# Kernel optimization log

Measured on AMD Instinct MI355X. Metric: run time of the kernel, lower is better.

## Reference

```python
import jax, jax.numpy as jnp
import numpy as np

D_MODEL, D_STATE, D_CONV, D_INNER, DT_RANK, K = 96, 16, 3, 192, 6, 4
B, H, W = 1, 64, 64


def setup_inputs() -> dict:
    key = jax.random.key(0)
    ks = jax.random.split(key, 10)
    x = jax.random.normal(ks[0], (B, H, W, D_MODEL), jnp.float32)
    in_proj_w = jax.random.normal(ks[1], (2 * D_INNER, D_MODEL), jnp.float32) * 0.02
    conv_w = jax.random.normal(ks[2], (D_INNER, 1, D_CONV, D_CONV), jnp.float32) * 0.1
    conv_b = jnp.zeros((D_INNER,), jnp.float32)
    x_proj_w = jax.random.normal(ks[3], (K, DT_RANK + 2 * D_STATE, D_INNER), jnp.float32) * 0.02
    dt_std = DT_RANK ** -0.5
    dt_w = jax.random.uniform(ks[4], (K, D_INNER, DT_RANK), jnp.float32, -dt_std, dt_std)
    # dt bias init: inv-softplus of dt ~ logUniform(1e-3, 1e-1)
    u = jax.random.uniform(ks[5], (K, D_INNER), jnp.float32)
    dt = jnp.exp(u * (np.log(0.1) - np.log(0.001)) + np.log(0.001)).clip(1e-4)
    dt_b = dt + jnp.log(-jnp.expm1(-dt))
    A_logs = jnp.log(jnp.broadcast_to(jnp.arange(1, D_STATE + 1, dtype=jnp.float32), (K * D_INNER, D_STATE)))
    Ds = jnp.ones((K * D_INNER,), jnp.float32)
    ln_g = jnp.ones((D_INNER,), jnp.float32)
    ln_b = jnp.zeros((D_INNER,), jnp.float32)
    out_proj_w = jax.random.normal(ks[6], (D_MODEL, D_INNER), jnp.float32) * 0.02
    return dict(x=x, in_proj_w=in_proj_w, conv_w=conv_w, conv_b=conv_b, x_proj_w=x_proj_w,
                dt_w=dt_w, dt_b=dt_b, A_logs=A_logs, Ds=Ds, ln_g=ln_g, ln_b=ln_b,
                out_proj_w=out_proj_w)


def _ss2d(x, in_proj_w, conv_w, conv_b, x_proj_w, dt_w, dt_b, A_logs, Ds, ln_g, ln_b, out_proj_w):
    b, h, w, c = x.shape
    L = h * w
    d = conv_w.shape[0]            # d_inner
    n = A_logs.shape[1]            # d_state
    r = dt_w.shape[2]              # dt_rank
    # in_proj + split
    xz = jnp.einsum('bhwc,ec->bhwe', x, in_proj_w)
    xx, z = xz[..., :d], xz[..., d:]
    # depthwise conv (NCHW) + SiLU
    xc = xx.transpose(0, 3, 1, 2)
    pad = (D_CONV - 1) // 2
    xc = jax.lax.conv_general_dilated(xc, conv_w, (1, 1), [(pad, pad), (pad, pad)],
                                      feature_group_count=d) + conv_b[None, :, None, None]
    xc = jax.nn.silu(xc)
    # 4 scan directions: HW, WH, and their reverses
    x_hw = xc.reshape(b, d, L)
    x_wh = xc.transpose(0, 1, 3, 2).reshape(b, d, L)
    xs = jnp.stack([x_hw, x_wh, x_hw[..., ::-1], x_wh[..., ::-1]], axis=1)  # (b,K,d,L)
    x_dbl = jnp.einsum('bkdl,kcd->bkcl', xs, x_proj_w)
    dts, Bs, Cs = x_dbl[:, :, :r], x_dbl[:, :, r:r + n], x_dbl[:, :, r + n:]
    dts = jnp.einsum('bkrl,kdr->bkdl', dts, dt_w)
    delta = jax.nn.softplus(dts + dt_b[None, :, :, None])        # (b,K,d,L)
    A = -jnp.exp(A_logs).reshape(K, d, n)
    # time-major scanned inputs
    dA = jnp.exp(jnp.einsum('bkdl,kdn->lbkdn', delta, A))        # (L,b,K,d,n)
    dBu = jnp.einsum('bkdl,bknl,bkdl->lbkdn', delta, Bs, xs)
    Ct = Cs.transpose(3, 0, 1, 2)                                # (L,b,K,n)
    def step(hst, inp):
        dA_t, dBu_t, C_t = inp
        hst = dA_t * hst + dBu_t
        return hst, jnp.einsum('bkdn,bkn->bkd', hst, C_t)
    h0 = jnp.zeros((b, K, d, n), jnp.float32)
    _, ys = jax.lax.scan(step, h0, (dA, dBu, Ct))                # ys: (L,b,K,d)
    out_y = ys.transpose(1, 2, 3, 0) + xs * Ds.reshape(K, d)[None, :, :, None]
    # recombine directions
    inv = out_y[:, 2:4][..., ::-1]
    y1 = out_y[:, 0]
    y2 = inv[:, 0]
    wh = out_y[:, 1].reshape(b, d, w, h).transpose(0, 1, 3, 2).reshape(b, d, L)
    invwh = inv[:, 1].reshape(b, d, w, h).transpose(0, 1, 3, 2).reshape(b, d, L)
    y = (y1 + y2 + wh + invwh).transpose(0, 2, 1).reshape(b, h, w, d)
    # LayerNorm (eps=1e-5, torch default)
    mu = y.mean(-1, keepdims=True)
    var = ((y - mu) ** 2).mean(-1, keepdims=True)
    y = (y - mu) * jax.lax.rsqrt(var + 1e-5) * ln_g + ln_b
    y = y * jax.nn.silu(z)
    return jnp.einsum('bhwd,cd->bhwc', y, out_proj_w)


def reference(x, in_proj_w, conv_w, conv_b, x_proj_w, dt_w, dt_b, A_logs, Ds, ln_g, ln_b, out_proj_w):
    return _ss2d(x, in_proj_w, conv_w, conv_b, x_proj_w, dt_w, dt_b, A_logs, Ds, ln_g, ln_b, out_proj_w)
```

## Files before the change

### kernel.cpp

```cpp
#include <hip/hip_runtime.h>
#include <hip/hip_bf16.h>

#define LL 4096
#define DM 96
#define DI 192
#define NS 16
#define RK 6
#define RKP 8
#define KD 4
#define CPROJ 38
#define NC (KD*DI*NS)
#define PT 32
#define WS 196
#define OT 16
#define L2E 1.44269504f

__device__ __forceinline__ float b2f(__hip_bfloat16 v){ return __bfloat162float(v); }

__device__ __forceinline__ int detect_bf16(const unsigned short* __restrict__ xh, int tid, int* sflag){
  if (tid < 64){
    unsigned short u = xh[2*tid];
    int e = (u >> 7) & 0xFF;
    int sane = (e >= 107 && e <= 131) ? 1 : 0;
    unsigned long long m = __ballot(sane);
    if (tid == 0) *sflag = (__popcll(m) >= 32) ? 1 : 0;
  }
  return 0;
}

struct P12 { const void* p[12]; };
__global__ void k_convert_all(P12 ptrs, float* __restrict__ dst) {
  const int off[13] = {0,393216,430080,431808,432000,461184,465792,466560,
                       478848,479616,479808,480000,498432};
  __shared__ int sflag;
  detect_bf16((const unsigned short*)ptrs.p[0], threadIdx.x, &sflag);
  __syncthreads();
  int f = sflag;
  int i = blockIdx.x * 256 + threadIdx.x;
  if (i >= 498432) return;
  int j = 0;
  #pragma unroll
  for (int s = 1; s < 12; s++) if (i >= off[s]) j = s;
  int e = i - off[j];
  if (f) dst[i] = b2f(((const __hip_bfloat16*)ptrs.p[j])[e]);
  else   dst[i] = ((const float*)ptrs.p[j])[e];
}

__global__ void k_inproj(const float* __restrict__ x,
                         const float* __restrict__ w,
                         float* __restrict__ xx, float* __restrict__ z) {
  __shared__ float xr[8*DM];
  int l0 = blockIdx.x * 8;
  int tid = threadIdx.x;
  for (int i = tid; i < 8*DM; i += 384) xr[i] = x[l0*DM + i];
  __syncthreads();
  int e = tid;
  float acc[8];
  #pragma unroll
  for (int i=0;i<8;i++) acc[i]=0.f;
  const float* wr = w + e*DM;
  for (int c=0;c<DM;c++){
    float wv = wr[c];
    #pragma unroll
    for (int i=0;i<8;i++) acc[i] = fmaf(wv, xr[i*DM+c], acc[i]);
  }
  if (e < DI) {
    #pragma unroll
    for (int i=0;i<8;i++) xx[(l0+i)*DI + e] = acc[i];
  } else {
    int e2 = e - DI;
    #pragma unroll
    for (int i=0;i<8;i++) z[(l0+i)*DI + e2] = acc[i];
  }
}

__global__ void k_conv(const float* __restrict__ xx,
                       const float* __restrict__ cw,
                       const float* __restrict__ cb,
                       float* __restrict__ xc,
                       float* __restrict__ xct) {
  int l = blockIdx.x;
  int d = threadIdx.x;
  int h = l >> 6, w = l & 63;
  float acc = cb[d];
  #pragma unroll
  for (int ki=0; ki<3; ki++){
    int hh = h + ki - 1;
    if ((unsigned)hh >= 64u) continue;
    #pragma unroll
    for (int kj=0;kj<3;kj++){
      int wj = w + kj - 1;
      if ((unsigned)wj >= 64u) continue;
      acc = fmaf(cw[d*9 + ki*3 + kj], xx[(hh*64+wj)*DI + d], acc);
    }
  }
  float v = acc / (1.f + __expf(-acc));
  xc[l*DI + d] = v;
  xct[(((w<<6)|h))*DI + d] = v;
}

__device__ __forceinline__ int dir_map(int k, int t){
  if (k==0) return t;
  if (k==1) return ((t&63)<<6) | (t>>6);
  if (k==2) return 4095 - t;
  int u = 4095 - t; return ((u&63)<<6) | (u>>6);
}

__global__ void __launch_bounds__(256) k_proj(const float* __restrict__ xc,
                       const float* __restrict__ xpw,
                       float* __restrict__ dts,
                       float* __restrict__ Bb, float* __restrict__ Cb,
                       float* __restrict__ yacc_hw, float* __restrict__ yacc_wh) {
  __shared__ float wl[CPROJ*WS];
  __shared__ float xs[PT*WS];
  int b = blockIdx.x;
  int k = b >> 7;
  int t_base = (b & 127) * PT;
  int tid = threadIdx.x;
  if (k < 2){
    float4* yz = (float4*)((k==0 ? yacc_hw : yacc_wh) + (size_t)t_base*DI);
    for (int idx = tid; idx < PT*DI/4; idx += 256)
      yz[idx] = make_float4(0.f,0.f,0.f,0.f);
  }
  for (int idx = tid; idx < CPROJ*DI; idx += 256){
    int cc = idx / DI, j = idx - cc*DI;
    wl[cc*WS + j] = xpw[(k*CPROJ + cc)*DI + j];
  }
  for (int idx = tid; idx < PT*DI; idx += 256){
    int tt = idx / DI, j = idx - tt*DI;
    xs[tt*WS + j] = xc[dir_map(k, t_base + tt)*DI + j];
  }
  __syncthreads();
  int tg = tid & 7;
  int ty = tid >> 3;
  int cc0 = ty;
  int has2 = (ty + 32 < CPROJ);
  int cc1 = has2 ? (ty + 32) : ty;
  float a0x=0.f,a0y=0.f,a0z=0.f,a0w=0.f;
  float a1x=0.f,a1y=0.f,a1z=0.f,a1w=0.f;
  const float4* w0p = (const float4*)&wl[cc0*WS];
  const float4* w1p = (const float4*)&wl[cc1*WS];
  const float4* x0p = (const float4*)&xs[(tg     )*WS];
  const float4* x1p = (const float4*)&xs[(tg +  8)*WS];
  const float4* x2p = (const float4*)&xs[(tg + 16)*WS];
  const float4* x3p = (const float4*)&xs[(tg + 24)*WS];
  #pragma unroll 4
  for (int jc = 0; jc < DI/4; jc++){
    float4 w0 = w0p[jc], w1 = w1p[jc];
    float4 x0 = x0p[jc], x1 = x1p[jc], x2 = x2p[jc], x3 = x3p[jc];
    a0x = fmaf(w0.x,x0.x,fmaf(w0.y,x0.y,fmaf(w0.z,x0.z,fmaf(w0.w,x0.w,a0x))));
    a0y = fmaf(w0.x,x1.x,fmaf(w0.y,x1.y,fmaf(w0.z,x1.z,fmaf(w0.w,x1.w,a0y))));
    a0z = fmaf(w0.x,x2.x,fmaf(w0.y,x2.y,fmaf(w0.z,x2.z,fmaf(w0.w,x2.w,a0z))));
    a0w = fmaf(w0.x,x3.x,fmaf(w0.y,x3.y,fmaf(w0.z,x3.z,fmaf(w0.w,x3.w,a0w))));
    a1x = fmaf(w1.x,x0.x,fmaf(w1.y,x0.y,fmaf(w1.z,x0.z,fmaf(w1.w,x0.w,a1x))));
    a1y = fmaf(w1.x,x1.x,fmaf(w1.y,x1.y,fmaf(w1.z,x1.z,fmaf(w1.w,x1.w,a1y))));
    a1z = fmaf(w1.x,x2.x,fmaf(w1.y,x2.y,fmaf(w1.z,x2.z,fmaf(w1.w,x2.w,a1z))));
    a1w = fmaf(w1.x,x3.x,fmaf(w1.y,x3.y,fmaf(w1.z,x3.z,fmaf(w1.w,x3.w,a1w))));
  }
  float accs0[4] = {a0x,a0y,a0z,a0w};
  float accs1[4] = {a1x,a1y,a1z,a1w};
  #pragma unroll
  for (int i=0;i<4;i++){
    int t = t_base + tg + 8*i;
    size_t kt = (size_t)k*LL + t;
    {
      int cc = cc0; float v = accs0[i];
      if (cc < RK)            dts[kt*RKP + cc] = v;
      else if (cc < RK+NS)    Bb [kt*NS + (cc-RK)] = v;
      else                    Cb [kt*NS + (cc-RK-NS)] = v;
    }
    if (has2){
      int cc = ty + 32; float v = accs1[i];
      if (cc < RK+NS)         Bb [kt*NS + (cc-RK)] = v;
      else                    Cb [kt*NS + (cc-RK-NS)] = v;
    }
  }
}

template<int CHB>
__global__ void __launch_bounds__(256) k_scan1(
                      const float* __restrict__ xc_hw,
                      const float* __restrict__ xc_wh,
                      const float* __restrict__ dts,
                      const float* __restrict__ Bbuf,
                      const float* __restrict__ Cbuf,
                      const float* __restrict__ A_logs,
                      const float* __restrict__ dtw,
                      const float* __restrict__ dtb,
                      float* __restrict__ Pb, float* __restrict__ Hb,
                      float* __restrict__ SDb,
                      float* __restrict__ yacc_hw, float* __restrict__ yacc_wh) {
  constexpr int CS = LL >> CHB;
  int b = blockIdx.x;
  int c = b & ((1<<CHB)-1);
  int kg = b >> CHB;
  int k = kg / 3, dg3 = kg - k*3;
  int tid = threadIdx.x;
  int dl = tid >> 2, nq = tid & 3;
  int d = dg3*64 + dl;
  int kd = k*DI + d;
  float4 Al = *(const float4*)&A_logs[kd*NS + nq*4];
  float A0 = -__expf(Al.x)*L2E, A1 = -__expf(Al.y)*L2E;
  float A2 = -__expf(Al.z)*L2E, A3 = -__expf(Al.w)*L2E;
  float bt = dtb[kd];
  float w0 = dtw[kd*RK+0], w1 = dtw[kd*RK+1], w2 = dtw[kd*RK+2];
  float w3 = dtw[kd*RK+3], w4 = dtw[kd*RK+4], w5 = dtw[kd*RK+5];
  const float* dr = dts + ((size_t)k*LL + c*CS)*RKP;
  const float4* bp = (const float4*)(Bbuf + ((size_t)k*LL + c*CS)*NS) + nq;
  const float4* cp = (const float4*)(Cbuf + ((size_t)k*LL + c*CS)*NS) + nq;
  const float* xbase = (k & 1) ? xc_wh : xc_hw;
  float* ybase = (k & 1) ? yacc_wh : yacc_hw;
  int l0 = (k < 2) ? (c*CS) : (4095 - c*CS);
  int lstep = (k < 2) ? DI : -DI;
  const float* xp = xbase + (size_t)l0*DI + d;
  float* yp = ybase + (size_t)l0*DI + d;
  float* sdp = SDb + ((size_t)k*LL + c*CS)*DI + d;
  float h0=0.f,h1=0.f,h2=0.f,h3=0.f, cumD=0.f;
  #pragma unroll
  for (int s=0; s<CS; s++){
    float4 lo = *(const float4*)(dr + s*RKP);
    float4 hi = *(const float4*)(dr + s*RKP + 4);
    float v = bt;
    v = fmaf(w0, lo.x, v); v = fmaf(w1, lo.y, v); v = fmaf(w2, lo.z, v);
    v = fmaf(w3, lo.w, v); v = fmaf(w4, hi.x, v); v = fmaf(w5, hi.y, v);
    float sp = (v > 20.f) ? v : __logf(1.f + __expf(v));
    cumD += sp;
    float sx = sp * xp[(ptrdiff_t)s*lstep];
    float4 bv = bp[s*4];
    float4 cv = cp[s*4];
    float a;
    a = exp2f(sp*A0); h0 = fmaf(a, h0, sx*bv.x);
    a = exp2f(sp*A1); h1 = fmaf(a, h1, sx*bv.y);
    a = exp2f(sp*A2); h2 = fmaf(a, h2, sx*bv.z);
    a = exp2f(sp*A3); h3 = fmaf(a, h3, sx*bv.w);
    float y = h0*cv.x + h1*cv.y + h2*cv.z + h3*cv.w;
    y += __shfl_xor(y, 1, 64);
    y += __shfl_xor(y, 2, 64);
    if (nq == 0){
      atomicAdd(&yp[(ptrdiff_t)s*lstep], y);
      sdp[s*DI] = cumD;
    }
  }
  int base = c*NC + kd*NS + nq*4;
  *(float4*)&Pb[base] = make_float4(exp2f(A0*cumD), exp2f(A1*cumD),
                                    exp2f(A2*cumD), exp2f(A3*cumD));
  *(float4*)&Hb[base] = make_float4(h0,h1,h2,h3);
}

template<int CHB>
__global__ void __launch_bounds__(256) k_scan2(
                      const float* __restrict__ Pb, float* __restrict__ Hb) {
  constexpr int CH = 1 << CHB;
  int idx = blockIdx.x*256 + threadIdx.x;
  float h = 0.f;
  #pragma unroll 8
  for (int c=0;c<CH;c++){
    float P = Pb[c*NC + idx];
    float Hc = Hb[c*NC + idx];
    Hb[c*NC + idx] = h;
    h = fmaf(P, h, Hc);
  }
}

template<int CHB>
__global__ void __launch_bounds__(192) k_corr(
                      const float* __restrict__ Cbuf,
                      const float* __restrict__ A_logs,
                      const float* __restrict__ Hb,
                      const float* __restrict__ SDb,
                      float* __restrict__ yacc_hw, float* __restrict__ yacc_wh) {
  constexpr int CS = LL >> CHB;
  int b = blockIdx.x;
  int k = b >> CHB;
  int c = b & ((1<<CHB)-1);
  if (c == 0) return;
  int t0 = c*CS;
  int d = threadIdx.x;
  int kd = k*DI + d;
  __shared__ float cs[CS*NS];
  for (int i = d; i < CS*NS; i += 192)
    cs[i] = Cbuf[((size_t)k*LL + t0)*NS + i];
  float A2[16], he[16];
  {
    const float4* ap = (const float4*)&A_logs[kd*NS];
    const float4* hp = (const float4*)&Hb[c*NC + kd*NS];
    #pragma unroll
    for (int i=0;i<4;i++){
      float4 av = ap[i];
      A2[4*i+0] = -__expf(av.x)*L2E; A2[4*i+1] = -__expf(av.y)*L2E;
      A2[4*i+2] = -__expf(av.z)*L2E; A2[4*i+3] = -__expf(av.w)*L2E;
      *(float4*)&he[4*i] = hp[i];
    }
  }
  __syncthreads();
  float* ybase = (k & 1) ? yacc_wh : yacc_hw;
  int l0 = (k < 2) ? t0 : (4095 - t0);
  int lstep = (k < 2) ? DI : -DI;
  float* yp = ybase + (size_t)l0*DI + d;
  const float* sdp = SDb + ((size_t)k*LL + t0)*DI + d;
  #pragma unroll 4
  for (int s=0; s<CS; s++){
    float SD = sdp[s*DI];
    float corr = 0.f;
    #pragma unroll
    for (int n=0;n<16;n++)
      corr = fmaf(cs[s*NS+n]*exp2f(A2[n]*SD), he[n], corr);
    atomicAdd(&yp[(ptrdiff_t)s*lstep], corr);
  }
}

__global__ void k_ln(const float* __restrict__ yacc_hw,
                     const float* __restrict__ yacc_wh,
                     const float* __restrict__ xc,
                     const float* __restrict__ z,
                     const float* __restrict__ Ds,
                     const float* __restrict__ ln_g,
                     const float* __restrict__ ln_b,
                     float* __restrict__ g) {
  int l = blockIdx.x;
  int d = threadIdx.x;
  int lt = ((l & 63) << 6) | (l >> 6);
  float y = yacc_hw[(size_t)l*DI + d] + yacc_wh[(size_t)lt*DI + d];
  float dsum = Ds[0*DI+d] + Ds[1*DI+d] + Ds[2*DI+d] + Ds[3*DI+d];
  y = fmaf(xc[l*DI+d], dsum, y);
  float s1 = y, s2 = y*y;
  #pragma unroll
  for (int off=32; off; off>>=1){
    s1 += __shfl_xor(s1, off, 64);
    s2 += __shfl_xor(s2, off, 64);
  }
  __shared__ float red[6];
  int wave = d >> 6;
  if ((d & 63) == 0){ red[wave] = s1; red[3+wave] = s2; }
  __syncthreads();
  float sum = red[0]+red[1]+red[2];
  float sq  = red[3]+red[4]+red[5];
  float mu = sum * (1.f/192.f);
  float var = sq * (1.f/192.f) - mu*mu;
  float rstd = rsqrtf(var + 1e-5f);
  float yn = (y - mu) * rstd * ln_g[d] + ln_b[d];
  float zv = z[l*DI + d];
  g[(size_t)l*DI + d] = yn * (zv / (1.f + __expf(-zv)));
}

__global__ void __launch_bounds__(192) k_oproj(const float* __restrict__ g,
                      const float* __restrict__ opw,
                      void* __restrict__ out,
                      const unsigned short* __restrict__ xh) {
  __shared__ float gs[OT*WS];
  __shared__ int sflag;
  int tid = threadIdx.x;
  detect_bf16(xh, tid, &sflag);
  int l0 = blockIdx.x * OT;
  const float4* gsrc = (const float4*)(g + (size_t)l0*DI);
  for (int idx = tid; idx < OT*DI/4; idx += 192){
    int row = idx / 48, col = idx - row*48;
    float4 v = gsrc[idx];
    *(float4*)&gs[row*WS + col*4] = v;
  }
  __syncthreads();
  int half = tid / 96;
  int e = tid - half*96;
  int r0 = half*8;
  float acc[8];
  #pragma unroll
  for (int i=0;i<8;i++) acc[i] = 0.f;
  const float4* wrow = (const float4*)(opw + e*DI);
  #pragma unroll 4
  for (int jc = 0; jc < DI/4; jc++){
    float4 w = wrow[jc];
    #pragma unroll
    for (int i=0;i<8;i++){
      float4 gv = *(const float4*)&gs[(r0+i)*WS + jc*4];
      acc[i] = fmaf(w.x,gv.x,fmaf(w.y,gv.y,fmaf(w.z,gv.z,fmaf(w.w,gv.w,acc[i]))));
    }
  }
  int f = sflag;
  #pragma unroll
  for (int i=0;i<8;i++){
    int l = l0 + r0 + i;
    if (f) ((__hip_bfloat16*)out)[l*DM + e] = __float2bfloat16(acc[i]);
    else   ((float*)out)[l*DM + e] = acc[i];
  }
}

extern "C" void kernel_launch(void* const* d_in, const int* in_sizes, int n_in,
                              void* d_out, int out_size, void* d_ws, size_t ws_size,
                              hipStream_t stream) {
  float* ws = (float*)d_ws;
  float* cvt = ws + 16;
  const int off[13] = {0,393216,430080,431808,432000,461184,465792,466560,
                       478848,479616,479808,480000,498432};
  float* c[12];
  for (int i = 0; i < 12; i++) c[i] = cvt + off[i];

  float* big    = cvt + 498432;
  float* xx     = big;
  float* z      = xx + (size_t)LL*DI;
  float* xc     = z  + (size_t)LL*DI;
  float* xct    = xc + (size_t)LL*DI;
  float* dts    = xct + (size_t)LL*DI;
  float* Bb     = dts + (size_t)KD*LL*RKP;
  float* Cb     = Bb + (size_t)KD*LL*NS;
  float* Pb     = Cb + (size_t)KD*LL*NS;
  size_t need256 = (size_t)(16 + 498432 + 4*786432 + 131072 + 2*262144
                            + 2*256*NC + (size_t)KD*LL*DI + 786432) * 4;
  int chBits = (ws_size >= need256) ? 8 : 6;
  int CHn = 1 << chBits;
  float* Hb      = Pb + (size_t)CHn*NC;
  float* SDb     = Hb + (size_t)CHn*NC;
  float* yacc_wh = SDb + (size_t)KD*LL*DI;
  float* yacc_hw = xx;

  P12 ptrs;
  for (int i = 0; i < 12; i++) ptrs.p[i] = d_in[i];
  k_convert_all<<<(498432 + 255)/256, 256, 0, stream>>>(ptrs, cvt);

  k_inproj<<<LL/8, 384, 0, stream>>>(c[0], c[1], xx, z);
  k_conv<<<LL, DI, 0, stream>>>(xx, c[2], c[3], xc, xct);
  k_proj<<<KD*(LL/PT), 256, 0, stream>>>(xc, c[4], dts, Bb, Cb, yacc_hw, yacc_wh);
  if (chBits == 8){
    k_scan1<8><<<KD*3*256, 256, 0, stream>>>(xc, xct, dts, Bb, Cb, c[7], c[5], c[6],
                                             Pb, Hb, SDb, yacc_hw, yacc_wh);
    k_scan2<8><<<NC/256, 256, 0, stream>>>(Pb, Hb);
    k_corr<8><<<KD*256, 192, 0, stream>>>(Cb, c[7], Hb, SDb, yacc_hw, yacc_wh);
  } else {
    k_scan1<6><<<KD*3*64, 256, 0, stream>>>(xc, xct, dts, Bb, Cb, c[7], c[5], c[6],
                                            Pb, Hb, SDb, yacc_hw, yacc_wh);
    k_scan2<6><<<NC/256, 256, 0, stream>>>(Pb, Hb);
    k_corr<6><<<KD*64, 192, 0, stream>>>(Cb, c[7], Hb, SDb, yacc_hw, yacc_wh);
  }
  k_ln<<<LL, DI, 0, stream>>>(yacc_hw, yacc_wh, xc, z, c[8], c[9], c[10], Hb);
  k_oproj<<<LL/OT, 192, 0, stream>>>(Hb, c[11], d_out, (const unsigned short*)d_in[0]);
}
```

Measured before the change: 207.8 us.

## Replace atomic scan accumulation with per-direction buffers and skip input conversion

```diff
diff --git a/kernel.cpp b/kernel.cpp
--- a/kernel.cpp
+++ b/kernel.cpp
@@ -30,29 +30,38 @@
 
 struct P12 { const void* p[12]; };
 __global__ void k_convert_all(P12 ptrs, float* __restrict__ dst) {
-  const int off[13] = {0,393216,430080,431808,432000,461184,465792,466560,
-                       478848,479616,479808,480000,498432};
+  const int off[12] = {0,36864,38592,38784,67968,72576,73344,85632,86400,86592,86784,105216};
   __shared__ int sflag;
   detect_bf16((const unsigned short*)ptrs.p[0], threadIdx.x, &sflag);
   __syncthreads();
   int f = sflag;
   int i = blockIdx.x * 256 + threadIdx.x;
-  if (i >= 498432) return;
+  if (i >= 105216) return;
   int j = 0;
   #pragma unroll
-  for (int s = 1; s < 12; s++) if (i >= off[s]) j = s;
+  for (int s = 1; s < 11; s++) if (i >= off[s]) j = s;
   int e = i - off[j];
-  if (f) dst[i] = b2f(((const __hip_bfloat16*)ptrs.p[j])[e]);
-  else   dst[i] = ((const float*)ptrs.p[j])[e];
-}
-
-__global__ void k_inproj(const float* __restrict__ x,
+  const void* src = ptrs.p[j+1];
+  if (f) dst[i] = b2f(((const __hip_bfloat16*)src)[e]);
+  else   dst[i] = ((const float*)src)[e];
+}
+
+__global__ void k_inproj(const void* __restrict__ xraw,
                          const float* __restrict__ w,
                          float* __restrict__ xx, float* __restrict__ z) {
   __shared__ float xr[8*DM];
+  __shared__ int sflag;
+  int tid = threadIdx.x;
+  detect_bf16((const unsigned short*)xraw, tid, &sflag);
+  __syncthreads();
   int l0 = blockIdx.x * 8;
-  int tid = threadIdx.x;
-  for (int i = tid; i < 8*DM; i += 384) xr[i] = x[l0*DM + i];
+  if (sflag){
+    const __hip_bfloat16* xb = (const __hip_bfloat16*)xraw + (size_t)l0*DM;
+    for (int i = tid; i < 8*DM; i += 384) xr[i] = b2f(xb[i]);
+  } else {
+    const float* xf = (const float*)xraw + (size_t)l0*DM;
+    for (int i = tid; i < 8*DM; i += 384) xr[i] = xf[i];
+  }
   __syncthreads();
   int e = tid;
   float acc[8];
@@ -109,19 +118,13 @@
 __global__ void __launch_bounds__(256) k_proj(const float* __restrict__ xc,
                        const float* __restrict__ xpw,
                        float* __restrict__ dts,
-                       float* __restrict__ Bb, float* __restrict__ Cb,
-                       float* __restrict__ yacc_hw, float* __restrict__ yacc_wh) {
+                       float* __restrict__ Bb, float* __restrict__ Cb) {
   __shared__ float wl[CPROJ*WS];
   __shared__ float xs[PT*WS];
   int b = blockIdx.x;
   int k = b >> 7;
   int t_base = (b & 127) * PT;
   int tid = threadIdx.x;
-  if (k < 2){
-    float4* yz = (float4*)((k==0 ? yacc_hw : yacc_wh) + (size_t)t_base*DI);
-    for (int idx = tid; idx < PT*DI/4; idx += 256)
-      yz[idx] = make_float4(0.f,0.f,0.f,0.f);
-  }
   for (int idx = tid; idx < CPROJ*DI; idx += 256){
     int cc = idx / DI, j = idx - cc*DI;
     wl[cc*WS + j] = xpw[(k*CPROJ + cc)*DI + j];
@@ -189,7 +192,7 @@
                       const float* __restrict__ dtb,
                       float* __restrict__ Pb, float* __restrict__ Hb,
                       float* __restrict__ SDb,
-                      float* __restrict__ yacc_hw, float* __restrict__ yacc_wh) {
+                      float* __restrict__ ydir) {
   constexpr int CS = LL >> CHB;
   int b = blockIdx.x;
   int c = b & ((1<<CHB)-1);
@@ -209,11 +212,10 @@
   const float4* bp = (const float4*)(Bbuf + ((size_t)k*LL + c*CS)*NS) + nq;
   const float4* cp = (const float4*)(Cbuf + ((size_t)k*LL + c*CS)*NS) + nq;
   const float* xbase = (k & 1) ? xc_wh : xc_hw;
-  float* ybase = (k & 1) ? yacc_wh : yacc_hw;
   int l0 = (k < 2) ? (c*CS) : (4095 - c*CS);
   int lstep = (k < 2) ? DI : -DI;
   const float* xp = xbase + (size_t)l0*DI + d;
-  float* yp = ybase + (size_t)l0*DI + d;
+  float* yp = ydir + ((size_t)k*LL + c*CS)*DI + d;
   float* sdp = SDb + ((size_t)k*LL + c*CS)*DI + d;
   float h0=0.f,h1=0.f,h2=0.f,h3=0.f, cumD=0.f;
   #pragma unroll
@@ -237,7 +239,7 @@
     y += __shfl_xor(y, 1, 64);
     y += __shfl_xor(y, 2, 64);
     if (nq == 0){
-      atomicAdd(&yp[(ptrdiff_t)s*lstep], y);
+      yp[s*DI] = y;
       sdp[s*DI] = cumD;
     }
   }
@@ -268,7 +270,7 @@
                       const float* __restrict__ A_logs,
                       const float* __restrict__ Hb,
                       const float* __restrict__ SDb,
-                      float* __restrict__ yacc_hw, float* __restrict__ yacc_wh) {
+                      float* __restrict__ ydir) {
   constexpr int CS = LL >> CHB;
   int b = blockIdx.x;
   int k = b >> CHB;
@@ -293,10 +295,7 @@
     }
   }
   __syncthreads();
-  float* ybase = (k & 1) ? yacc_wh : yacc_hw;
-  int l0 = (k < 2) ? t0 : (4095 - t0);
-  int lstep = (k < 2) ? DI : -DI;
-  float* yp = ybase + (size_t)l0*DI + d;
+  float* yp = ydir + ((size_t)k*LL + t0)*DI + d;
   const float* sdp = SDb + ((size_t)k*LL + t0)*DI + d;
   #pragma unroll 4
   for (int s=0; s<CS; s++){
@@ -305,12 +304,11 @@
     #pragma unroll
     for (int n=0;n<16;n++)
       corr = fmaf(cs[s*NS+n]*exp2f(A2[n]*SD), he[n], corr);
-    atomicAdd(&yp[(ptrdiff_t)s*lstep], corr);
-  }
-}
-
-__global__ void k_ln(const float* __restrict__ yacc_hw,
-                     const float* __restrict__ yacc_wh,
+    yp[s*DI] += corr;
+  }
+}
+
+__global__ void k_ln(const float* __restrict__ ydir,
                      const float* __restrict__ xc,
                      const float* __restrict__ z,
                      const float* __restrict__ Ds,
@@ -320,7 +318,10 @@
   int l = blockIdx.x;
   int d = threadIdx.x;
   int lt = ((l & 63) << 6) | (l >> 6);
-  float y = yacc_hw[(size_t)l*DI + d] + yacc_wh[(size_t)lt*DI + d];
+  float y = ydir[(size_t)l*DI + d]
+          + ydir[((size_t)LL   + lt)*DI + d]
+          + ydir[((size_t)2*LL + (4095 - l))*DI + d]
+          + ydir[((size_t)3*LL + (4095 - lt))*DI + d];
   float dsum = Ds[0*DI+d] + Ds[1*DI+d] + Ds[2*DI+d] + Ds[3*DI+d];
   y = fmaf(xc[l*DI+d], dsum, y);
   float s1 = y, s2 = y*y;
@@ -389,12 +390,12 @@
                               hipStream_t stream) {
   float* ws = (float*)d_ws;
   float* cvt = ws + 16;
-  const int off[13] = {0,393216,430080,431808,432000,461184,465792,466560,
-                       478848,479616,479808,480000,498432};
+  const int off[12] = {0,36864,38592,38784,67968,72576,73344,85632,86400,86592,86784,105216};
   float* c[12];
-  for (int i = 0; i < 12; i++) c[i] = cvt + off[i];
-
-  float* big    = cvt + 498432;
+  c[0] = nullptr;
+  for (int i = 1; i < 12; i++) c[i] = cvt + off[i-1];
+
+  float* big    = cvt + 105216;
   float* xx     = big;
   float* z      = xx + (size_t)LL*DI;
   float* xc     = z  + (size_t)LL*DI;
@@ -403,33 +404,33 @@
   float* Bb     = dts + (size_t)KD*LL*RKP;
   float* Cb     = Bb + (size_t)KD*LL*NS;
   float* Pb     = Cb + (size_t)KD*LL*NS;
-  size_t need256 = (size_t)(16 + 498432 + 4*786432 + 131072 + 2*262144
-                            + 2*256*NC + (size_t)KD*LL*DI + 786432) * 4;
+  size_t need256 = (size_t)(16 + 105216 + 4*786432 + 131072 + 2*262144
+                            + 2*256*NC + 2*(size_t)KD*LL*DI) * 4;
   int chBits = (ws_size >= need256) ? 8 : 6;
   int CHn = 1 << chBits;
-  float* Hb      = Pb + (size_t)CHn*NC;
-  float* SDb     = Hb + (size_t)CHn*NC;
-  float* yacc_wh = SDb + (size_t)KD*LL*DI;
-  float* yacc_hw = xx;
+  float* Hb   = Pb + (size_t)CHn*NC;
+  float* SDb  = Hb + (size_t)CHn*NC;
+  float* ydir = SDb + (size_t)KD*LL*DI;
+  float* g    = Pb;
 
   P12 ptrs;
   for (int i = 0; i < 12; i++) ptrs.p[i] = d_in[i];
-  k_convert_all<<<(498432 + 255)/256, 256, 0, stream>>>(ptrs, cvt);
-
-  k_inproj<<<LL/8, 384, 0, stream>>>(c[0], c[1], xx, z);
+  k_convert_all<<<(105216 + 255)/256, 256, 0, stream>>>(ptrs, cvt);
+
+  k_inproj<<<LL/8, 384, 0, stream>>>(d_in[0], c[1], xx, z);
   k_conv<<<LL, DI, 0, stream>>>(xx, c[2], c[3], xc, xct);
-  k_proj<<<KD*(LL/PT), 256, 0, stream>>>(xc, c[4], dts, Bb, Cb, yacc_hw, yacc_wh);
+  k_proj<<<KD*(LL/PT), 256, 0, stream>>>(xc, c[4], dts, Bb, Cb);
   if (chBits == 8){
     k_scan1<8><<<KD*3*256, 256, 0, stream>>>(xc, xct, dts, Bb, Cb, c[7], c[5], c[6],
-                                             Pb, Hb, SDb, yacc_hw, yacc_wh);
+                                             Pb, Hb, SDb, ydir);
     k_scan2<8><<<NC/256, 256, 0, stream>>>(Pb, Hb);
-    k_corr<8><<<KD*256, 192, 0, stream>>>(Cb, c[7], Hb, SDb, yacc_hw, yacc_wh);
+    k_corr<8><<<KD*256, 192, 0, stream>>>(Cb, c[7], Hb, SDb, ydir);
   } else {
     k_scan1<6><<<KD*3*64, 256, 0, stream>>>(xc, xct, dts, Bb, Cb, c[7], c[5], c[6],
-                                            Pb, Hb, SDb, yacc_hw, yacc_wh);
+                                            Pb, Hb, SDb, ydir);
     k_scan2<6><<<NC/256, 256, 0, stream>>>(Pb, Hb);
-    k_corr<6><<<KD*64, 192, 0, stream>>>(Cb, c[7], Hb, SDb, yacc_hw, yacc_wh);
-  }
-  k_ln<<<LL, DI, 0, stream>>>(yacc_hw, yacc_wh, xc, z, c[8], c[9], c[10], Hb);
-  k_oproj<<<LL/OT, 192, 0, stream>>>(Hb, c[11], d_out, (const unsigned short*)d_in[0]);
-}
+    k_corr<6><<<KD*64, 192, 0, stream>>>(Cb, c[7], Hb, SDb, ydir);
+  }
+  k_ln<<<LL, DI, 0, stream>>>(ydir, xc, z, c[8], c[9], c[10], g);
+  k_oproj<<<LL/OT, 192, 0, stream>>>(g, c[11], d_out, (const unsigned short*)d_in[0]);
+}
```

Measured after the change: 209.4 us. Within noise of the previous version (+0.8%).
